# Kernel tuning notes

Measured on AMD Instinct MI355X. Metric: run time of the kernel, lower is better.

## Reference

```python
import jax, jax.numpy as jnp
import numpy as np

DIM = 192; HEADS = 6; WS = (2, 7, 7); SS = (1, 3, 3)
HEAD_DIM = DIM // HEADS; SCALE = HEAD_DIM ** -0.5
NW_TOK = WS[0] * WS[1] * WS[2]  # 98 tokens per window
HIDDEN = 4 * DIM


def _rel_pos_index():
    d, h, w = WS
    coords = np.stack(np.meshgrid(np.arange(d), np.arange(h), np.arange(w), indexing='ij'))
    cf = coords.reshape(3, -1)
    rc = (cf[:, :, None] - cf[:, None, :]).transpose(1, 2, 0).astype(np.int64)
    rc[:, :, 0] += d - 1; rc[:, :, 1] += h - 1; rc[:, :, 2] += w - 1
    rc[:, :, 0] *= (2 * h - 1) * (2 * w - 1)
    rc[:, :, 1] *= (2 * w - 1)
    return jnp.asarray(rc.sum(-1))  # (98, 98)

REL_IDX = _rel_pos_index()


def layer_norm(x, w, b):
    m = x.mean(-1, keepdims=True)
    v = ((x - m) ** 2).mean(-1, keepdims=True)
    return (x - m) / jnp.sqrt(v + 1e-5) * w + b


def window_partition(x, ws):
    B, D, H, W, C = x.shape
    x = x.reshape(B, D // ws[0], ws[0], H // ws[1], ws[1], W // ws[2], ws[2], C)
    x = x.transpose(0, 1, 3, 5, 2, 4, 6, 7)
    return x.reshape(-1, ws[0] * ws[1] * ws[2], C)


def window_reverse(w, ws, B, D, H, W):
    x = w.reshape(B, D // ws[0], H // ws[1], W // ws[2], ws[0], ws[1], ws[2], -1)
    x = x.transpose(0, 1, 4, 2, 5, 3, 6, 7)
    return x.reshape(B, D, H, W, -1)


def mlp(x, fc1_w, fc1_b, fc2_w, fc2_b):
    return jax.nn.gelu(x @ fc1_w + fc1_b, approximate=False) @ fc2_w + fc2_b


def setup_inputs() -> dict:
    key = jax.random.key(0)
    ks = jax.random.split(key, 16)
    B, D, H, W, C = 2, 8, 56, 56, DIM
    nW = (D // WS[0]) * (H // WS[1]) * (W // WS[2])
    return {
        'x': jax.random.normal(ks[0], (B, D, H, W, C), jnp.float32),
        'global_token': jax.random.normal(ks[1], (B * nW, 1, C), jnp.float32),
        'position': jax.random.normal(ks[2], (B * nW, 1, C), jnp.float32),
        'attn_mask': jax.random.normal(ks[3], (nW, NW_TOK, NW_TOK), jnp.float32),
        'norm1_w': jnp.ones((C,), jnp.float32),
        'norm1_b': jnp.zeros((C,), jnp.float32),
        'qkv_w': jax.random.normal(ks[4], (C, 3 * C), jnp.float32) * 0.02,
        'qkv_b': jnp.zeros((3 * C,), jnp.float32),
        'proj_w': jax.random.normal(ks[5], (C, C), jnp.float32) * 0.02,
        'proj_b': jnp.zeros((C,), jnp.float32),
        'rpb_table': jax.random.normal(ks[6], ((2 * WS[0] - 1) * (2 * WS[1] - 1) * (2 * WS[2] - 1), HEADS), jnp.float32) * 0.02,
        'norm2_w': jnp.ones((C,), jnp.float32),
        'norm2_b': jnp.zeros((C,), jnp.float32),
        'fc1_w': jax.random.normal(ks[7], (C, HIDDEN), jnp.float32) * 0.02,
        'fc1_b': jnp.zeros((HIDDEN,), jnp.float32),
        'fc2_w': jax.random.normal(ks[8], (HIDDEN, C), jnp.float32) * 0.02,
        'fc2_b': jnp.zeros((C,), jnp.float32),
    }


def reference(x, global_token, position, attn_mask, norm1_w, norm1_b, qkv_w, qkv_b,
              proj_w, proj_b, rpb_table, norm2_w, norm2_b, fc1_w, fc1_b, fc2_w, fc2_b):
    B, D, H, W, C = x.shape
    shortcut = x
    xn = layer_norm(x, norm1_w, norm1_b)
    # pad to multiple of window size (static no-op here but kept for fidelity)
    pd, ph, pw = (-D) % WS[0], (-H) % WS[1], (-W) % WS[2]
    xn = jnp.pad(xn, ((0, 0), (0, pd), (0, ph), (0, pw), (0, 0)))
    Dp, Hp, Wp = D + pd, H + ph, W + pw
    xn = jnp.roll(xn, (-SS[0], -SS[1], -SS[2]), axis=(1, 2, 3))
    xw = window_partition(xn, WS)                       # (B*nW, 98, C)
    xw = jnp.concatenate([global_token, xw], axis=1)    # (B*nW, 99, C)
    B_, N, _ = xw.shape
    qkv = (xw @ qkv_w + qkv_b).reshape(B_, N, 3, HEADS, HEAD_DIM).transpose(2, 0, 3, 1, 4)
    q, k, v = qkv[0] * SCALE, qkv[1], qkv[2]
    attn = jnp.einsum('bhnd,bhmd->bhnm', q, k)          # (B_, H, 99, 99)
    rpb = rpb_table[REL_IDX.reshape(-1)].reshape(NW_TOK, NW_TOK, HEADS).transpose(2, 0, 1)
    nW = attn_mask.shape[0]
    extra = rpb[None] + jnp.tile(attn_mask, (B_ // nW, 1, 1))[:, None]
    attn = attn.at[:, :, 1:, 1:].add(extra)
    attn = jax.nn.softmax(attn, axis=-1)
    out = jnp.einsum('bhnm,bhmd->bhnd', attn, v).transpose(0, 2, 1, 3).reshape(B_, N, C)
    out = out @ proj_w + proj_b
    xw, gt = out[:, 1:], out[:, :1]
    xr = window_reverse(xw, WS, B, Dp, Hp, Wp)
    xr = jnp.roll(xr, SS, axis=(1, 2, 3))[:, :D, :H, :W, :]
    x = shortcut + xr
    x = x + mlp(layer_norm(x, norm2_w, norm2_b), fc1_w, fc1_b, fc2_w, fc2_b)
    gt = gt + mlp(layer_norm(gt, norm2_w, norm2_b), fc1_w, fc1_b, fc2_w, fc2_b)
    return (x, gt)
```

## Files before the change

### kernel.cpp

```cpp
#include <hip/hip_runtime.h>
#include <math.h>

typedef float f32x4 __attribute__((ext_vector_type(4)));
typedef __bf16 bf16x4 __attribute__((ext_vector_type(4)));
typedef __bf16 bf16x8 __attribute__((ext_vector_type(8)));

union FragU { bf16x8 v; bf16x4 h[2]; };

__device__ __forceinline__ unsigned short f2bf(float x) {
  union { float f; unsigned u; } un; un.f = x;
  unsigned r = un.u + 0x7FFFu + ((un.u >> 16) & 1u);
  return (unsigned short)(r >> 16);
}
__device__ __forceinline__ float bf2f(unsigned short h) {
  union { unsigned u; float f; } un; un.u = ((unsigned)h) << 16;
  return un.f;
}

__device__ __forceinline__ void gl16(const unsigned short* g, unsigned short* l) {
  __builtin_amdgcn_global_load_lds(
      (const __attribute__((address_space(1))) void*)g,
      (__attribute__((address_space(3))) void*)l, 16, 0, 0);
}

#define MROWS 50688
#define XTOK  50176
#define GT_OFF 9633792
#define SCALE_Q 0.17677669529663687f

__global__ __launch_bounds__(256) void prep_w(
    const float* __restrict__ qkvw, const float* __restrict__ projw,
    const float* __restrict__ fc1w, const float* __restrict__ fc2w,
    unsigned short* __restrict__ out)
{
  int idx = blockIdx.x * 256 + threadIdx.x;
  float v;
  if (idx < 110592)      { int n = idx / 192, k = idx - n * 192; v = qkvw[k * 576 + n]; }
  else if (idx < 147456) { int j = idx - 110592; int n = j / 192, k = j - n * 192; v = projw[k * 192 + n]; }
  else if (idx < 294912) { int j = idx - 147456; int n = j / 192, k = j - n * 192; v = fc1w[k * 768 + n]; }
  else                   { int j = idx - 294912; int n = j / 768, k = j - n * 768; v = fc2w[k * 192 + n]; }
  out[idx] = f2bf(v);
}

__global__ __launch_bounds__(256) void prep_maskT(
    const float* __restrict__ amask, unsigned int* __restrict__ maskP)
{
  __shared__ float M[98][99];
  const int tid = threadIdx.x, w256 = blockIdx.x;
  const float* src = amask + (size_t)w256 * 9604;
  for (int i = tid; i < 9604; i += 256) {
    int ti = i / 98, tj = i - ti * 98;
    M[ti][tj] = src[i];
  }
  __syncthreads();
  unsigned int* dst = maskP + (size_t)w256 * 6336;
  for (int o = tid; o < 6336; o += 256) {
    int base = o / 396, rem = o - base * 396;
    int t = rem / 99, r = rem - t * 99;
    int c0 = base + 32 * t;
    unsigned int res = 0;
    #pragma unroll
    for (int h = 0; h < 2; h++) {
      int c = c0 + 16 * h;
      float v = 0.0f;
      if (r >= 1 && c >= 1 && c <= 98) v = M[r - 1][c - 1];
      res |= ((unsigned int)f2bf(v)) << (16 * h);
    }
    dst[o] = res;
  }
}

__global__ __launch_bounds__(256) void prep_rpbT(
    const float* __restrict__ rpb, unsigned int* __restrict__ rpbP)
{
  int idx = blockIdx.x * 256 + threadIdx.x;
  if (idx >= 38016) return;
  int head = idx / 6336, o = idx - head * 6336;
  int base = o / 396, rem = o - base * 396;
  int t = rem / 99, r = rem - t * 99;
  int c0 = base + 32 * t;
  unsigned int res = 0;
  #pragma unroll
  for (int h = 0; h < 2; h++) {
    int c = c0 + 16 * h;
    float v = 0.0f;
    if (r >= 1 && c >= 1 && c <= 98) {
      int ti = r - 1, tj = c - 1;
      int tdi = ti / 49, ri = ti - tdi * 49, thi = ri / 7, twi = ri - thi * 7;
      int tdj = tj / 49, rj = tj - tdj * 49, thj = rj / 7, twj = rj - thj * 7;
      int rel = (tdi - tdj + 1) * 169 + (thi - thj + 6) * 13 + (twi - twj + 6);
      v = rpb[rel * 6 + head];
    }
    res |= ((unsigned int)f2bf(v)) << (16 * h);
  }
  rpbP[idx] = res;
}

__global__ __launch_bounds__(256) void ln1_kernel(
    const float* __restrict__ x, const float* __restrict__ gtok,
    const float* __restrict__ lw, const float* __restrict__ lb,
    unsigned short* __restrict__ out)
{
  int row = blockIdx.x * 4 + (threadIdx.x >> 6);
  int lane = threadIdx.x & 63;
  int win = row / 99, t = row - win * 99;
  size_t obase = (size_t)row * 192;
  if (t == 0) {
    const float* src = gtok + (size_t)win * 192;
    out[obase + lane]       = f2bf(src[lane]);
    out[obase + lane + 64]  = f2bf(src[lane + 64]);
    out[obase + lane + 128] = f2bf(src[lane + 128]);
    return;
  }
  int b = win >> 8, wi = win & 255;
  int wd = wi >> 6, wh = (wi >> 3) & 7, ww = wi & 7;
  int tt = t - 1, td = tt / 49, rr = tt - td * 49, th = rr / 7, tw = rr - th * 7;
  int d = (wd * 2 + td + 1) & 7;
  int h = wh * 7 + th + 3; if (h >= 56) h -= 56;
  int wc = ww * 7 + tw + 3; if (wc >= 56) wc -= 56;
  const float* src = x + ((size_t)(((b * 8 + d) * 56 + h) * 56 + wc)) * 192;
  float v0 = src[lane], v1 = src[lane + 64], v2 = src[lane + 128];
  float s = v0 + v1 + v2;
  float ss = v0 * v0 + v1 * v1 + v2 * v2;
  #pragma unroll
  for (int off = 32; off; off >>= 1) { s += __shfl_xor(s, off); ss += __shfl_xor(ss, off); }
  float mean = s * (1.0f / 192.0f);
  float var = ss * (1.0f / 192.0f) - mean * mean;
  float rstd = rsqrtf(var + 1e-5f);
  out[obase + lane]       = f2bf((v0 - mean) * rstd * lw[lane]       + lb[lane]);
  out[obase + lane + 64]  = f2bf((v1 - mean) * rstd * lw[lane + 64]  + lb[lane + 64]);
  out[obase + lane + 128] = f2bf((v2 - mean) * rstd * lw[lane + 128] + lb[lane + 128]);
}

__global__ __launch_bounds__(256) void ln2_kernel(
    const float* __restrict__ resbuf,
    const float* __restrict__ lw, const float* __restrict__ lb,
    unsigned short* __restrict__ out)
{
  int row = blockIdx.x * 4 + (threadIdx.x >> 6);
  int lane = threadIdx.x & 63;
  const float* src = resbuf + (size_t)row * 192;
  float v0 = src[lane], v1 = src[lane + 64], v2 = src[lane + 128];
  float s = v0 + v1 + v2;
  float ss = v0 * v0 + v1 * v1 + v2 * v2;
  #pragma unroll
  for (int off = 32; off; off >>= 1) { s += __shfl_xor(s, off); ss += __shfl_xor(ss, off); }
  float mean = s * (1.0f / 192.0f);
  float var = ss * (1.0f / 192.0f) - mean * mean;
  float rstd = rsqrtf(var + 1e-5f);
  size_t obase = (size_t)row * 192;
  out[obase + lane]       = f2bf((v0 - mean) * rstd * lw[lane]       + lb[lane]);
  out[obase + lane + 64]  = f2bf((v1 - mean) * rstd * lw[lane + 64]  + lb[lane + 64]);
  out[obase + lane + 128] = f2bf((v2 - mean) * rstd * lw[lane + 128] + lb[lane + 128]);
}

template<int MODE>
__global__ __launch_bounds__(256) void gemm_tpl(
    const unsigned short* __restrict__ A,
    const unsigned short* __restrict__ BT,
    const float* __restrict__ bias,
    unsigned short* __restrict__ outb,
    const float* __restrict__ xin,
    float* __restrict__ resbuf,
    float* __restrict__ dout,
    int N, int K, int NC, int NWG)
{
  __shared__ unsigned short As[128 * 64];
  __shared__ unsigned short Bs[64 * 64];
  const int tid = threadIdx.x, lane = tid & 63, w = tid >> 6;
  const int wm = w >> 1, wn = w & 1;
  const int l15 = lane & 15, l4 = lane >> 4;
  const int sx = lane & 7;
  const int srow8 = lane >> 3;
  const int csrc = (lane & 7) ^ srow8;

  const int L = blockIdx.x;
  const int xcd = L & 7, hi = L >> 3;
  const int q = NWG >> 3, rr = NWG & 7;
  const int wgid = (xcd < rr ? xcd * (q + 1) : rr * (q + 1) + (xcd - rr) * q) + hi;
  const int cb = wgid % NC, rb = wgid / NC;
  const int mbase = rb * 128, nbase = cb * 64;

  f32x4 acc[4][2] = {};

  const int kiters = K >> 6;
  for (int t = 0; t < kiters; t++) {
    const int kb = t * 64;
    #pragma unroll
    for (int i = 0; i < 4; i++) {
      int chunk = w * 4 + i;
      int row = chunk * 8 + srow8;
      gl16(A + (size_t)(mbase + row) * K + kb + csrc * 8, As + chunk * 512);
    }
    #pragma unroll
    for (int i = 0; i < 2; i++) {
      int chunk = w * 2 + i;
      int row = chunk * 8 + srow8;
      gl16(BT + (size_t)(nbase + row) * K + kb + csrc * 8, Bs + chunk * 512);
    }
    __syncthreads();

    #pragma unroll
    for (int ks = 0; ks < 2; ks++) {
      bf16x8 af[4], bfr[2];
      #pragma unroll
      for (int mi = 0; mi < 4; mi++) {
        int r = wm * 64 + mi * 16 + l15;
        af[mi] = *reinterpret_cast<const bf16x8*>(As + r * 64 + (((ks * 4 + l4) ^ sx) * 8));
      }
      #pragma unroll
      for (int nj = 0; nj < 2; nj++) {
        int c = wn * 32 + nj * 16 + l15;
        bfr[nj] = *reinterpret_cast<const bf16x8*>(Bs + c * 64 + (((ks * 4 + l4) ^ sx) * 8));
      }
      #pragma unroll
      for (int mi = 0; mi < 4; mi++)
        #pragma unroll
        for (int nj = 0; nj < 2; nj++)
          acc[mi][nj] = __builtin_amdgcn_mfma_f32_16x16x32_bf16(af[mi], bfr[nj], acc[mi][nj], 0, 0, 0);
    }
    if (t + 1 < kiters) __syncthreads();
  }

  #pragma unroll
  for (int mi = 0; mi < 4; mi++)
    #pragma unroll
    for (int nj = 0; nj < 2; nj++)
      #pragma unroll
      for (int reg = 0; reg < 4; reg++) {
        int r = mbase + wm * 64 + mi * 16 + l4 * 4 + reg;
        int c = nbase + wn * 32 + nj * 16 + l15;
        float v = acc[mi][nj][reg] + bias[c];
        if constexpr (MODE == 0) {
          if (c < 192) v *= SCALE_Q;
          outb[(size_t)r * N + c] = f2bf(v);
        } else if constexpr (MODE == 1) {
          int win = r / 99, t2 = r - win * 99;
          if (t2 == 0) {
            resbuf[(size_t)(XTOK + win) * 192 + c] = v;
          } else {
            int b = win >> 8, wi = win & 255;
            int wd = wi >> 6, wh = (wi >> 3) & 7, ww = wi & 7;
            int tt = t2 - 1, td = tt / 49, rr2 = tt - td * 49, th = rr2 / 7, tw = rr2 - th * 7;
            int d = (wd * 2 + td + 1) & 7;
            int h = wh * 7 + th + 3; if (h >= 56) h -= 56;
            int wc = ww * 7 + tw + 3; if (wc >= 56) wc -= 56;
            size_t idx = ((size_t)(((b * 8 + d) * 56 + h) * 56 + wc)) * 192 + c;
            resbuf[idx] = xin[idx] + v;
          }
        } else if constexpr (MODE == 2) {
          float p = v * (1.5957691216f + 0.0713548128f * v * v);
          float g = v * __builtin_amdgcn_rcpf(1.0f + __expf(-p));
          outb[(size_t)r * N + c] = f2bf(g);
        } else {
          v += resbuf[(size_t)r * 192 + c];
          if (r < XTOK) dout[(size_t)r * 192 + c] = v;
          else dout[GT_OFF + (size_t)(r - XTOK) * 192 + c] = v;
        }
      }
}

__global__ __launch_bounds__(256, 4) void attn_kernel(
    const unsigned short* __restrict__ qkv,
    const unsigned int* __restrict__ maskP,
    const unsigned int* __restrict__ rpbP,
    unsigned short* __restrict__ out)
{
  const int win = blockIdx.x & 511;
  const int head = blockIdx.x >> 9;
  const int tid = threadIdx.x, lane = tid & 63, w = tid >> 6;
  const int l15 = lane & 15, l4 = (lane >> 4) & 3;

  __shared__ __align__(16) unsigned short Qs[128][40];
  __shared__ __align__(16) unsigned short Ks[128][40];
  __shared__ __align__(16) unsigned short VTs[32][136];

  const size_t rowbase = (size_t)win * 99;

  const unsigned int* mkb = maskP + (size_t)(win & 255) * 6336;
  const unsigned int* rpb_ = rpbP + (size_t)head * 6336;
  const int q0 = w * 16 + l15;
  const int q1 = 64 + q0;
  const int r1 = q1 < 99 ? q1 : 0;
  unsigned int mk0[4][4], mk1[4][4], rp0[4][4], rp1[4][4];
  #pragma unroll
  for (int reg = 0; reg < 4; reg++)
    #pragma unroll
    for (int t = 0; t < 4; t++) {
      int boff = ((l4 * 4 + reg) * 4 + t) * 99;
      mk0[reg][t] = mkb[boff + q0];
      mk1[reg][t] = mkb[boff + r1];
      rp0[reg][t] = rpb_[boff + q0];
      rp1[reg][t] = rpb_[boff + r1];
    }

  for (int idx = tid; idx < 512; idx += 256) {
    int r = idx >> 2, seg = (idx & 3) * 8;
    int4 zq = {0,0,0,0}, zk = {0,0,0,0}, zv = {0,0,0,0};
    if (r < 99) {
      const unsigned short* src = qkv + (rowbase + r) * 576 + head * 32 + seg;
      zq = *reinterpret_cast<const int4*>(src);
      zk = *reinterpret_cast<const int4*>(src + 192);
      zv = *reinterpret_cast<const int4*>(src + 384);
    }
    *reinterpret_cast<int4*>(&Qs[r][seg]) = zq;
    *reinterpret_cast<int4*>(&Ks[r][seg]) = zk;
    const unsigned short* pv = reinterpret_cast<const unsigned short*>(&zv);
    #pragma unroll
    for (int j = 0; j < 8; j++) VTs[seg + j][r] = pv[j];
  }
  __syncthreads();

  f32x4 oacc[2][2] = {};

  #pragma unroll
  for (int qi = 0; qi < 2; qi++) {
    const int qrow = qi * 64 + w * 16 + l15;
    FragU qf;
    qf.h[0] = *reinterpret_cast<const bf16x4*>(&Qs[qrow][l4 * 4]);
    qf.h[1] = *reinterpret_cast<const bf16x4*>(&Qs[qrow][16 + l4 * 4]);

    f32x4 sacc[7] = {};
    #pragma unroll
    for (int nj = 0; nj < 7; nj++) {
      FragU kf;
      kf.h[0] = *reinterpret_cast<const bf16x4*>(&Ks[nj * 16 + l15][l4 * 4]);
      kf.h[1] = *reinterpret_cast<const bf16x4*>(&Ks[nj * 16 + l15][16 + l4 * 4]);
      sacc[nj] = __builtin_amdgcn_mfma_f32_16x16x32_bf16(kf.v, qf.v, sacc[nj], 0, 0, 0);
    }

    float m = -1e30f;
    #pragma unroll
    for (int nj = 0; nj < 7; nj++) {
      int t = nj >> 1;
      #pragma unroll
      for (int reg = 0; reg < 4; reg++) {
        unsigned int mu = qi ? mk1[reg][t] : mk0[reg][t];
        unsigned int ru = qi ? rp1[reg][t] : rp0[reg][t];
        unsigned int mb = (nj & 1) ? (mu & 0xFFFF0000u) : (mu << 16);
        unsigned int rb = (nj & 1) ? (ru & 0xFFFF0000u) : (ru << 16);
        float s = sacc[nj][reg] + __uint_as_float(mb) + __uint_as_float(rb);
        if (nj == 6 && (96 + l4 * 4 + reg) >= 99) s = -1e30f;
        sacc[nj][reg] = s;
        m = fmaxf(m, s);
      }
    }
    m = fmaxf(m, __shfl_xor(m, 16));
    m = fmaxf(m, __shfl_xor(m, 32));
    float sum = 0.0f;
    #pragma unroll
    for (int nj = 0; nj < 7; nj++)
      #pragma unroll
      for (int reg = 0; reg < 4; reg++) {
        float e = __expf(sacc[nj][reg] - m);
        sacc[nj][reg] = e;
        sum += e;
      }
    sum += __shfl_xor(sum, 16);
    sum += __shfl_xor(sum, 32);
    const float inv = 1.0f / sum;

    #pragma unroll
    for (int ks = 0; ks < 4; ks++) {
      union { unsigned short u[8]; bf16x8 v; } pa;
      #pragma unroll
      for (int j = 0; j < 4; j++) {
        pa.u[j] = f2bf(sacc[2 * ks][j] * inv);
        pa.u[4 + j] = (ks == 3) ? (unsigned short)0 : f2bf(sacc[2 * ks + 1][j] * inv);
      }
      #pragma unroll
      for (int njd = 0; njd < 2; njd++) {
        FragU vb;
        vb.h[0] = *reinterpret_cast<const bf16x4*>(&VTs[njd * 16 + l15][ks * 32 + l4 * 4]);
        vb.h[1] = *reinterpret_cast<const bf16x4*>(&VTs[njd * 16 + l15][ks * 32 + 16 + l4 * 4]);
        oacc[qi][njd] = __builtin_amdgcn_mfma_f32_16x16x32_bf16(pa.v, vb.v, oacc[qi][njd], 0, 0, 0);
      }
    }
  }

  #pragma unroll
  for (int qi = 0; qi < 2; qi++)
    #pragma unroll
    for (int njd = 0; njd < 2; njd++)
      #pragma unroll
      for (int reg = 0; reg < 4; reg++) {
        int q = qi * 64 + w * 16 + l4 * 4 + reg;
        if (q < 99)
          out[(rowbase + q) * 192 + head * 32 + njd * 16 + l15] = f2bf(oacc[qi][njd][reg]);
      }
}

extern "C" void kernel_launch(void* const* d_in, const int* in_sizes, int n_in,
                              void* d_out, int out_size, void* d_ws, size_t ws_size,
                              hipStream_t stream) {
  (void)in_sizes; (void)n_in; (void)out_size; (void)ws_size;
  const float* x     = (const float*)d_in[0];
  const float* gtok  = (const float*)d_in[1];
  const float* amask = (const float*)d_in[3];
  const float* n1w   = (const float*)d_in[4];
  const float* n1b   = (const float*)d_in[5];
  const float* qkvw  = (const float*)d_in[6];
  const float* qkvb  = (const float*)d_in[7];
  const float* projw = (const float*)d_in[8];
  const float* projb = (const float*)d_in[9];
  const float* rpb   = (const float*)d_in[10];
  const float* n2w   = (const float*)d_in[11];
  const float* n2b   = (const float*)d_in[12];
  const float* fc1w  = (const float*)d_in[13];
  const float* fc1b  = (const float*)d_in[14];
  const float* fc2w  = (const float*)d_in[15];
  const float* fc2b  = (const float*)d_in[16];

  char* ws = (char*)d_ws;
  unsigned short* wbuf = (unsigned short*)ws;
  unsigned short* X    = (unsigned short*)(ws + 884736);
  unsigned short* Qb   = (unsigned short*)(ws + 20348928);
  float*          Rb   = (float*)(ws + 98205696);
  unsigned int*   maskP= (unsigned int*)(ws + 98205696);
  unsigned int*   rpbP = (unsigned int*)(ws + 104693760);
  float* dout = (float*)d_out;

  prep_w<<<1728, 256, 0, stream>>>(qkvw, projw, fc1w, fc2w, wbuf);
  prep_maskT<<<256, 256, 0, stream>>>(amask, maskP);
  prep_rpbT<<<149, 256, 0, stream>>>(rpb, rpbP);
  ln1_kernel<<<12672, 256, 0, stream>>>(x, gtok, n1w, n1b, X);
  gemm_tpl<0><<<3564, 256, 0, stream>>>(X, wbuf, qkvb, Qb, nullptr, nullptr, nullptr, 576, 192, 9, 3564);
  attn_kernel<<<3072, 256, 0, stream>>>(Qb, maskP, rpbP, X);
  gemm_tpl<1><<<1188, 256, 0, stream>>>(X, wbuf + 110592, projb, nullptr, x, Rb, nullptr, 192, 192, 3, 1188);
  ln2_kernel<<<12672, 256, 0, stream>>>(Rb, n2w, n2b, X);
  gemm_tpl<2><<<4752, 256, 0, stream>>>(X, wbuf + 147456, fc1b, Qb, nullptr, nullptr, nullptr, 768, 192, 12, 4752);
  gemm_tpl<3><<<1188, 256, 0, stream>>>(Qb, wbuf + 294912, fc2b, nullptr, nullptr, Rb, dout, 192, 768, 3, 1188);
}
```

Baseline: 193.2 us.

## Double-buffer GEMM LDS tiles and merge prep kernels into one launch

The GEMM template now uses two LDS buffers for A and B and issues the global-to-LDS loads for the next K tile before running the MFMAs on the current one, so load latency can overlap compute. The three small preprocessing kernels (weight cast, mask packing, rpb packing) are folded into one launch that dispatches by block index, removing two launches. The cost is double the LDS per block, which may reduce occupancy. The loop still has a single barrier per iteration and no explicit wait on the asynchronous LDS loads for the next buffer, so correctness depends on how those loads are fenced.

```diff
diff --git a/kernel.cpp b/kernel.cpp
--- a/kernel.cpp
+++ b/kernel.cpp
@@ -28,33 +28,51 @@
 #define GT_OFF 9633792
 #define SCALE_Q 0.17677669529663687f
 
-__global__ __launch_bounds__(256) void prep_w(
+__global__ __launch_bounds__(256) void prep_all(
     const float* __restrict__ qkvw, const float* __restrict__ projw,
     const float* __restrict__ fc1w, const float* __restrict__ fc2w,
-    unsigned short* __restrict__ out)
-{
-  int idx = blockIdx.x * 256 + threadIdx.x;
-  float v;
-  if (idx < 110592)      { int n = idx / 192, k = idx - n * 192; v = qkvw[k * 576 + n]; }
-  else if (idx < 147456) { int j = idx - 110592; int n = j / 192, k = j - n * 192; v = projw[k * 192 + n]; }
-  else if (idx < 294912) { int j = idx - 147456; int n = j / 192, k = j - n * 192; v = fc1w[k * 768 + n]; }
-  else                   { int j = idx - 294912; int n = j / 768, k = j - n * 768; v = fc2w[k * 192 + n]; }
-  out[idx] = f2bf(v);
-}
-
-__global__ __launch_bounds__(256) void prep_maskT(
-    const float* __restrict__ amask, unsigned int* __restrict__ maskP)
+    const float* __restrict__ amask, const float* __restrict__ rpb,
+    unsigned short* __restrict__ wout,
+    unsigned int* __restrict__ maskP, unsigned int* __restrict__ rpbP)
 {
   __shared__ float M[98][99];
-  const int tid = threadIdx.x, w256 = blockIdx.x;
-  const float* src = amask + (size_t)w256 * 9604;
-  for (int i = tid; i < 9604; i += 256) {
-    int ti = i / 98, tj = i - ti * 98;
-    M[ti][tj] = src[i];
-  }
-  __syncthreads();
-  unsigned int* dst = maskP + (size_t)w256 * 6336;
-  for (int o = tid; o < 6336; o += 256) {
+  const int tid = threadIdx.x;
+  const int blk = blockIdx.x;
+  if (blk < 1728) {
+    int idx = blk * 256 + tid;
+    float v;
+    if (idx < 110592)      { int n = idx / 192, k = idx - n * 192; v = qkvw[k * 576 + n]; }
+    else if (idx < 147456) { int j = idx - 110592; int n = j / 192, k = j - n * 192; v = projw[k * 192 + n]; }
+    else if (idx < 294912) { int j = idx - 147456; int n = j / 192, k = j - n * 192; v = fc1w[k * 768 + n]; }
+    else                   { int j = idx - 294912; int n = j / 768, k = j - n * 768; v = fc2w[k * 192 + n]; }
+    wout[idx] = f2bf(v);
+  } else if (blk < 1984) {
+    const int w256 = blk - 1728;
+    const float* src = amask + (size_t)w256 * 9604;
+    for (int i = tid; i < 9604; i += 256) {
+      int ti = i / 98, tj = i - ti * 98;
+      M[ti][tj] = src[i];
+    }
+    __syncthreads();
+    unsigned int* dst = maskP + (size_t)w256 * 6336;
+    for (int o = tid; o < 6336; o += 256) {
+      int base = o / 396, rem = o - base * 396;
+      int t = rem / 99, r = rem - t * 99;
+      int c0 = base + 32 * t;
+      unsigned int res = 0;
+      #pragma unroll
+      for (int h = 0; h < 2; h++) {
+        int c = c0 + 16 * h;
+        float v = 0.0f;
+        if (r >= 1 && c >= 1 && c <= 98) v = M[r - 1][c - 1];
+        res |= ((unsigned int)f2bf(v)) << (16 * h);
+      }
+      dst[o] = res;
+    }
+  } else {
+    int idx = (blk - 1984) * 256 + tid;
+    if (idx >= 38016) return;
+    int head = idx / 6336, o = idx - head * 6336;
     int base = o / 396, rem = o - base * 396;
     int t = rem / 99, r = rem - t * 99;
     int c0 = base + 32 * t;
@@ -63,37 +81,17 @@
     for (int h = 0; h < 2; h++) {
       int c = c0 + 16 * h;
       float v = 0.0f;
-      if (r >= 1 && c >= 1 && c <= 98) v = M[r - 1][c - 1];
+      if (r >= 1 && c >= 1 && c <= 98) {
+        int ti = r - 1, tj = c - 1;
+        int tdi = ti / 49, ri = ti - tdi * 49, thi = ri / 7, twi = ri - thi * 7;
+        int tdj = tj / 49, rj = tj - tdj * 49, thj = rj / 7, twj = rj - thj * 7;
+        int rel = (tdi - tdj + 1) * 169 + (thi - thj + 6) * 13 + (twi - twj + 6);
+        v = rpb[rel * 6 + head];
+      }
       res |= ((unsigned int)f2bf(v)) << (16 * h);
     }
-    dst[o] = res;
+    rpbP[idx] = res;
   }
-}
-
-__global__ __launch_bounds__(256) void prep_rpbT(
-    const float* __restrict__ rpb, unsigned int* __restrict__ rpbP)
-{
-  int idx = blockIdx.x * 256 + threadIdx.x;
-  if (idx >= 38016) return;
-  int head = idx / 6336, o = idx - head * 6336;
-  int base = o / 396, rem = o - base * 396;
-  int t = rem / 99, r = rem - t * 99;
-  int c0 = base + 32 * t;
-  unsigned int res = 0;
-  #pragma unroll
-  for (int h = 0; h < 2; h++) {
-    int c = c0 + 16 * h;
-    float v = 0.0f;
-    if (r >= 1 && c >= 1 && c <= 98) {
-      int ti = r - 1, tj = c - 1;
-      int tdi = ti / 49, ri = ti - tdi * 49, thi = ri / 7, twi = ri - thi * 7;
-      int tdj = tj / 49, rj = tj - tdj * 49, thj = rj / 7, twj = rj - thj * 7;
-      int rel = (tdi - tdj + 1) * 169 + (thi - thj + 6) * 13 + (twi - twj + 6);
-      v = rpb[rel * 6 + head];
-    }
-    res |= ((unsigned int)f2bf(v)) << (16 * h);
-  }
-  rpbP[idx] = res;
 }
 
 __global__ __launch_bounds__(256) void ln1_kernel(
@@ -165,8 +163,8 @@
     float* __restrict__ dout,
     int N, int K, int NC, int NWG)
 {
-  __shared__ unsigned short As[128 * 64];
-  __shared__ unsigned short Bs[64 * 64];
+  __shared__ unsigned short As0[128 * 64], As1[128 * 64];
+  __shared__ unsigned short Bs0[64 * 64],  Bs1[64 * 64];
   const int tid = threadIdx.x, lane = tid & 63, w = tid >> 6;
   const int wm = w >> 1, wn = w & 1;
   const int l15 = lane & 15, l4 = lane >> 4;
@@ -181,24 +179,36 @@
   const int cb = wgid % NC, rb = wgid / NC;
   const int mbase = rb * 128, nbase = cb * 64;
 
+  const unsigned short* aSrc[4];
+  #pragma unroll
+  for (int i = 0; i < 4; i++)
+    aSrc[i] = A + (size_t)(mbase + (w * 4 + i) * 8 + srow8) * K + csrc * 8;
+  const unsigned short* bSrc[2];
+  #pragma unroll
+  for (int i = 0; i < 2; i++)
+    bSrc[i] = BT + (size_t)(nbase + (w * 2 + i) * 8 + srow8) * K + csrc * 8;
+
   f32x4 acc[4][2] = {};
 
   const int kiters = K >> 6;
+  #pragma unroll
+  for (int i = 0; i < 4; i++) gl16(aSrc[i], As0 + (w * 4 + i) * 512);
+  #pragma unroll
+  for (int i = 0; i < 2; i++) gl16(bSrc[i], Bs0 + (w * 2 + i) * 512);
+  __syncthreads();
+
   for (int t = 0; t < kiters; t++) {
-    const int kb = t * 64;
-    #pragma unroll
-    for (int i = 0; i < 4; i++) {
-      int chunk = w * 4 + i;
-      int row = chunk * 8 + srow8;
-      gl16(A + (size_t)(mbase + row) * K + kb + csrc * 8, As + chunk * 512);
-    }
-    #pragma unroll
-    for (int i = 0; i < 2; i++) {
-      int chunk = w * 2 + i;
-      int row = chunk * 8 + srow8;
-      gl16(BT + (size_t)(nbase + row) * K + kb + csrc * 8, Bs + chunk * 512);
-    }
-    __syncthreads();
+    unsigned short* aCur = (t & 1) ? As1 : As0;
+    unsigned short* bCur = (t & 1) ? Bs1 : Bs0;
+    if (t + 1 < kiters) {
+      unsigned short* aNxt = (t & 1) ? As0 : As1;
+      unsigned short* bNxt = (t & 1) ? Bs0 : Bs1;
+      const int kb = (t + 1) * 64;
+      #pragma unroll
+      for (int i = 0; i < 4; i++) gl16(aSrc[i] + kb, aNxt + (w * 4 + i) * 512);
+      #pragma unroll
+      for (int i = 0; i < 2; i++) gl16(bSrc[i] + kb, bNxt + (w * 2 + i) * 512);
+    }
 
     #pragma unroll
     for (int ks = 0; ks < 2; ks++) {
@@ -206,12 +216,12 @@
       #pragma unroll
       for (int mi = 0; mi < 4; mi++) {
         int r = wm * 64 + mi * 16 + l15;
-        af[mi] = *reinterpret_cast<const bf16x8*>(As + r * 64 + (((ks * 4 + l4) ^ sx) * 8));
+        af[mi] = *reinterpret_cast<const bf16x8*>(aCur + r * 64 + (((ks * 4 + l4) ^ sx) * 8));
       }
       #pragma unroll
       for (int nj = 0; nj < 2; nj++) {
         int c = wn * 32 + nj * 16 + l15;
-        bfr[nj] = *reinterpret_cast<const bf16x8*>(Bs + c * 64 + (((ks * 4 + l4) ^ sx) * 8));
+        bfr[nj] = *reinterpret_cast<const bf16x8*>(bCur + c * 64 + (((ks * 4 + l4) ^ sx) * 8));
       }
       #pragma unroll
       for (int mi = 0; mi < 4; mi++)
@@ -420,9 +430,7 @@
   unsigned int*   rpbP = (unsigned int*)(ws + 104693760);
   float* dout = (float*)d_out;
 
-  prep_w<<<1728, 256, 0, stream>>>(qkvw, projw, fc1w, fc2w, wbuf);
-  prep_maskT<<<256, 256, 0, stream>>>(amask, maskP);
-  prep_rpbT<<<149, 256, 0, stream>>>(rpb, rpbP);
+  prep_all<<<2133, 256, 0, stream>>>(qkvw, projw, fc1w, fc2w, amask, rpb, wbuf, maskP, rpbP);
   ln1_kernel<<<12672, 256, 0, stream>>>(x, gtok, n1w, n1b, X);
   gemm_tpl<0><<<3564, 256, 0, stream>>>(X, wbuf, qkvb, Qb, nullptr, nullptr, nullptr, 576, 192, 9, 3564);
   attn_kernel<<<3072, 256, 0, stream>>>(Qb, maskP, rpbP, X);
```

Measured after the change: 197.9 us. 1.02x slower.
